# Optimization experiments

Hardware: AMD Instinct MI355X
Metric: run time of the kernel (lower is better)

Reference implementation:

```python
import jax, jax.numpy as jnp
import numpy as np

N_PFAS, N_GW, N_SW = 20000, 100000, 20000
D_IN, D_OUT = 64, 128
E_PG, E_GP, E_SP, E_PS = 1600000, 1600000, 400000, 400000


def setup_inputs() -> dict:
    key = jax.random.key(0)
    ks = jax.random.split(key, 32)
    nrm = lambda k, shp, s=1.0: jax.random.normal(k, shp, jnp.float32) * s
    W = 0.05  # weight init scale
    inp = {
        # node features
        "x_pfas": nrm(ks[0], (N_PFAS, D_IN)),
        "x_gw": nrm(ks[1], (N_GW, D_IN)),
        "x_sw": nrm(ks[2], (N_SW, D_IN)),
        # edge indices per relation (src, dst)
        "ei_pg_src": jax.random.randint(ks[3], (E_PG,), 0, N_PFAS),
        "ei_pg_dst": jax.random.randint(ks[4], (E_PG,), 0, N_GW),
        "ei_gp_src": jax.random.randint(ks[5], (E_GP,), 0, N_GW),
        "ei_gp_dst": jax.random.randint(ks[6], (E_GP,), 0, N_PFAS),
        "ei_sp_src": jax.random.randint(ks[7], (E_SP,), 0, N_SW),
        "ei_sp_dst": jax.random.randint(ks[8], (E_SP,), 0, N_PFAS),
        "ei_ps_src": jax.random.randint(ks[9], (E_PS,), 0, N_PFAS),
        "ei_ps_dst": jax.random.randint(ks[10], (E_PS,), 0, N_SW),
        # SAGEConv params per relation: lin_l (neighbors, with bias), lin_r (root, no bias)
        "Wl_pg": nrm(ks[11], (D_IN, D_OUT), W), "Wr_pg": nrm(ks[12], (D_IN, D_OUT), W), "b_pg": jnp.zeros((D_OUT,), jnp.float32),
        "Wl_gp": nrm(ks[13], (D_IN, D_OUT), W), "Wr_gp": nrm(ks[14], (D_IN, D_OUT), W), "b_gp": jnp.zeros((D_OUT,), jnp.float32),
        "Wl_sp": nrm(ks[15], (D_IN, D_OUT), W), "Wr_sp": nrm(ks[16], (D_IN, D_OUT), W), "b_sp": jnp.zeros((D_OUT,), jnp.float32),
        "Wl_ps": nrm(ks[17], (D_IN, D_OUT), W), "Wr_ps": nrm(ks[18], (D_IN, D_OUT), W), "b_ps": jnp.zeros((D_OUT,), jnp.float32),
        # final linear head + PReLU
        "W_lin": nrm(ks[19], (D_OUT, 1), W), "b_lin": jnp.zeros((1,), jnp.float32),
        "alpha": jnp.full((1,), 0.25, jnp.float32),
    }
    return inp


def _sage(x_src, x_dst, src, dst, Wl, Wr, b, n_dst):
    # PyG SAGEConv: out = lin_l(mean_{j in N(i)} x_j) + lin_r(x_i)
    msg = x_src[src]                                   # [E, D_in] gather
    agg = jax.ops.segment_sum(msg, dst, num_segments=n_dst)        # [n_dst, D_in]
    cnt = jax.ops.segment_sum(jnp.ones(src.shape, x_src.dtype), dst, num_segments=n_dst)
    mean = agg / jnp.maximum(cnt, 1.0)[:, None]
    return mean @ Wl + x_dst @ Wr + b


def _prelu(y, a):
    return jnp.where(y > 0, y, a * y)


def reference(x_pfas, x_gw, x_sw, ei_pg_src, ei_pg_dst, ei_gp_src, ei_gp_dst,
              ei_sp_src, ei_sp_dst, ei_ps_src, ei_ps_dst,
              Wl_pg, Wr_pg, b_pg, Wl_gp, Wr_gp, b_gp, Wl_sp, Wr_sp, b_sp,
              Wl_ps, Wr_ps, b_ps, W_lin, b_lin, alpha):
    # HeteroConv with aggr='sum': pfas_sites receives from two relations (summed)
    h_gw = jax.nn.relu(_sage(x_pfas, x_gw, ei_pg_src, ei_pg_dst, Wl_pg, Wr_pg, b_pg, N_GW))
    h_pfas = jax.nn.relu(
        _sage(x_gw, x_pfas, ei_gp_src, ei_gp_dst, Wl_gp, Wr_gp, b_gp, N_PFAS)
        + _sage(x_sw, x_pfas, ei_sp_src, ei_sp_dst, Wl_sp, Wr_sp, b_sp, N_PFAS))
    h_sw = jax.nn.relu(_sage(x_pfas, x_sw, ei_ps_src, ei_ps_dst, Wl_ps, Wr_ps, b_ps, N_SW))
    out_gw = _prelu(h_gw @ W_lin + b_lin, alpha)   # [N_GW, 1]
    out_sw = _prelu(h_sw @ W_lin + b_lin, alpha)   # [N_SW, 1]
    return (h_pfas, out_gw, out_sw)
```

## Files before the change

### kernel.cpp

```cpp
#include <hip/hip_runtime.h>
#include <hip/hip_bf16.h>

#define N_PFAS 20000
#define N_GW   100000
#define N_SW   20000
#define N_SEG  160000
#define BASE_GW 0
#define BASE_GP 100000
#define BASE_SP 120000
#define BASE_PS 140000
#define NBIN 1250
#define NB_FILL 512
#define SORT_CAP 12288
#define STAGE_CAP 8192
#define N_XROW 140000

typedef __attribute__((ext_vector_type(8))) short short8;
typedef __attribute__((ext_vector_type(4))) float f32x4;
typedef __attribute__((ext_vector_type(2))) float f32x2;

__device__ __forceinline__ unsigned short f2bf(float f) {
    union { float f; unsigned int u; } v;
    v.f = f;
    unsigned int u = v.u;
    unsigned int r = (u + 0x7fffu + ((u >> 16) & 1u)) >> 16;
    return (unsigned short)r;
}

#if __has_builtin(__builtin_amdgcn_cvt_pk_f32_fp8) && __has_builtin(__builtin_amdgcn_cvt_pk_fp8_f32)
#define FP8_HW 1
__device__ __forceinline__ unsigned int enc_fp8x4(float4 v) {
    int r = __builtin_amdgcn_cvt_pk_fp8_f32(v.x, v.y, 0, false);
    r = __builtin_amdgcn_cvt_pk_fp8_f32(v.z, v.w, r, true);
    return (unsigned int)r;
}
__device__ __forceinline__ void dec_fp8x4v(unsigned int u, f32x2& lo, f32x2& hi) {
    lo = __builtin_amdgcn_cvt_pk_f32_fp8(u, false);
    hi = __builtin_amdgcn_cvt_pk_f32_fp8(u, true);
}
#else
__device__ __forceinline__ unsigned char enc1_e5m2(float f) {
    union { unsigned short u; _Float16 h; } cv;
    cv.h = (_Float16)f;
    unsigned int u = cv.u;
    unsigned int r = (u + 0x7Fu + ((u >> 8) & 1u)) >> 8;
    return (unsigned char)(r > 255u ? 255u : r);
}
__device__ __forceinline__ unsigned int enc_fp8x4(float4 v) {
    return (unsigned int)enc1_e5m2(v.x) | ((unsigned int)enc1_e5m2(v.y) << 8)
         | ((unsigned int)enc1_e5m2(v.z) << 16) | ((unsigned int)enc1_e5m2(v.w) << 24);
}
__device__ __forceinline__ float dec1_e5m2(unsigned int b) {
    union { unsigned short u; _Float16 h; } cv;
    cv.u = (unsigned short)(b << 8);
    return (float)cv.h;
}
__device__ __forceinline__ void dec_fp8x4v(unsigned int u, f32x2& lo, f32x2& hi) {
    lo.x = dec1_e5m2(u & 0xFF); lo.y = dec1_e5m2((u >> 8) & 0xFF);
    hi.x = dec1_e5m2((u >> 16) & 0xFF); hi.y = dec1_e5m2(u >> 24);
}
#endif

__device__ __forceinline__ void edge_lookup(int i,
    const int* __restrict__ s0, const int* __restrict__ d0, int E0,
    const int* __restrict__ s1, const int* __restrict__ d1, int E1,
    const int* __restrict__ s2, const int* __restrict__ d2, int E2,
    const int* __restrict__ s3, const int* __restrict__ d3,
    int& g, int& sv)
{
    if (i < E0)                { g = BASE_GW + d0[i];                 sv = s0 ? s0[i] : 0; }
    else if (i < E0 + E1)      { int j = i - E0;           g = BASE_GP + d1[j]; sv = s1 ? s1[j] : 0; }
    else if (i < E0 + E1 + E2) { int j = i - E0 - E1;      g = BASE_SP + d2[j]; sv = s2 ? s2[j] : 0; }
    else                       { int j = i - E0 - E1 - E2; g = BASE_PS + d3[j]; sv = s3 ? s3[j] : 0; }
}

__global__ void __launch_bounds__(1024)
count_cast(const int* __restrict__ d0, int E0, const int* __restrict__ d1, int E1,
           const int* __restrict__ d2, int E2, const int* __restrict__ d3, int E3,
           const float* __restrict__ xp, const float* __restrict__ xg,
           const float* __restrict__ xs, unsigned short* __restrict__ x16,
           unsigned int* __restrict__ x8, int* __restrict__ countMat)
{
    const int T0 = 20000 * 16, T1 = 120000 * 16, TT = N_XROW * 16;
    for (int i = blockIdx.x * 1024 + threadIdx.x; i < TT; i += NB_FILL * 1024) {
        float4 v;
        if (i < T0)      v = ((const float4*)xp)[i];
        else if (i < T1) v = ((const float4*)xg)[i - T0];
        else             v = ((const float4*)xs)[i - T1];
        ushort4 o;
        o.x = f2bf(v.x); o.y = f2bf(v.y); o.z = f2bf(v.z); o.w = f2bf(v.w);
        ((ushort4*)x16)[i] = o;
        x8[i] = enc_fp8x4(v);
    }

    __shared__ int h[4][NBIN];
    for (int i = threadIdx.x; i < NBIN; i += 1024) {
        h[0][i] = 0; h[1][i] = 0; h[2][i] = 0; h[3][i] = 0;
    }
    __syncthreads();
    int sub = threadIdx.x & 3;
    int total = E0 + E1 + E2 + E3;
    int CH = (total + NB_FILL - 1) / NB_FILL;
    int s = blockIdx.x * CH;
    int e = s + CH; if (e > total) e = total;
    for (int i0 = s + threadIdx.x * 4; i0 < e; i0 += 1024 * 4) {
        int gs[4];
        int m = e - i0; if (m > 4) m = 4;
        #pragma unroll
        for (int u = 0; u < 4; u++) {
            if (u < m) {
                int g, sv;
                edge_lookup(i0 + u, nullptr, d0, E0, nullptr, d1, E1,
                            nullptr, d2, E2, nullptr, d3, g, sv);
                gs[u] = g;
            }
        }
        #pragma unroll
        for (int u = 0; u < 4; u++)
            if (u < m) atomicAdd(&h[sub][gs[u] >> 7], 1);
    }
    __syncthreads();
    for (int i = threadIdx.x; i < NBIN; i += 1024)
        countMat[blockIdx.x * NBIN + i] = h[0][i] + h[1][i] + h[2][i] + h[3][i];
}

__global__ void __launch_bounds__(1024)
scan_rows(const int* __restrict__ countMat, int* __restrict__ lofs)
{
    __shared__ int lds[2048];
    int k = blockIdx.x;
    int t = threadIdx.x;
    int v0 = (t < NBIN) ? countMat[k * NBIN + t] : 0;
    int v1 = (t + 1024 < NBIN) ? countMat[k * NBIN + t + 1024] : 0;
    lds[t] = v0; lds[t + 1024] = v1;
    __syncthreads();
    #pragma unroll
    for (int off = 1; off < 2048; off <<= 1) {
        int a = (t >= off) ? lds[t - off] : 0;
        int b = (t + 1024 >= off) ? lds[t + 1024 - off] : 0;
        __syncthreads();
        lds[t] += a; lds[t + 1024] += b;
        __syncthreads();
    }
    if (t < NBIN) lofs[k * NBIN + t] = lds[t] - v0;
    if (t + 1024 < NBIN) lofs[k * NBIN + t + 1024] = lds[t + 1024] - v1;
}

__global__ void __launch_bounds__(1024)
fill_stage(const int* __restrict__ s0, const int* __restrict__ d0, int E0,
           const int* __restrict__ s1, const int* __restrict__ d1, int E1,
           const int* __restrict__ s2, const int* __restrict__ d2, int E2,
           const int* __restrict__ s3, const int* __restrict__ d3, int E3,
           const int* __restrict__ lofs, int* __restrict__ eb)
{
    __shared__ int cur[NBIN];
    __shared__ int stage[STAGE_CAP];
    int k = blockIdx.x;
    for (int i = threadIdx.x; i < NBIN; i += 1024) cur[i] = lofs[k * NBIN + i];
    __syncthreads();
    int total = E0 + E1 + E2 + E3;
    int CH = (total + NB_FILL - 1) / NB_FILL;
    int s = k * CH;
    int e = s + CH; if (e > total) e = total;
    for (int i0 = s + threadIdx.x * 4; i0 < e; i0 += 1024 * 4) {
        int g[4], sv[4];
        int m = e - i0; if (m > 4) m = 4;
        #pragma unroll
        for (int u = 0; u < 4; u++)
            if (u < m) edge_lookup(i0 + u, s0, d0, E0, s1, d1, E1,
                                   s2, d2, E2, s3, d3, g[u], sv[u]);
        #pragma unroll
        for (int u = 0; u < 4; u++) {
            if (u < m) {
                int slot = atomicAdd(&cur[g[u] >> 7], 1);
                stage[slot] = sv[u] | ((g[u] & 127) << 20);
            }
        }
    }
    __syncthreads();
    int n = e - s;
    for (int i = threadIdx.x; i < n; i += 1024) eb[s + i] = stage[i];
}

__global__ void __launch_bounds__(1024)
sort_agg(const int* __restrict__ countMat, const int* __restrict__ lofs,
         const int* __restrict__ eb, const unsigned int* __restrict__ x8,
         unsigned short* __restrict__ meanAll, int E_total)
{
    __shared__ int stage[SORT_CAP];
    __shared__ unsigned short perm[SORT_CAP];
    __shared__ int rs[NB_FILL];
    __shared__ int cposS[NB_FILL + 1];
    __shared__ int cnt[128], basep[128], cur[128], lstart[128];
    int lane = threadIdx.x & 63;
    int t = threadIdx.x;
    int b = (int)((blockIdx.x + 781u) % NBIN);
    int CH = (E_total + NB_FILL - 1) / NB_FILL;

    if (t < 128) cnt[t] = 0;
    if (t < NB_FILL) {
        int ckv = countMat[t * NBIN + b];
        rs[t] = t * CH + lofs[t * NBIN + b];
        cposS[t + 1] = ckv;
    }
    if (t == 0) cposS[0] = 0;
    __syncthreads();
    #pragma unroll
    for (int off = 1; off < NB_FILL; off <<= 1) {
        int v = 0;
        if (t < NB_FILL && t >= off) v = cposS[t + 1 - off];
        __syncthreads();
        if (t < NB_FILL) cposS[t + 1] += v;
        __syncthreads();
    }
    int n = cposS[NB_FILL];
    if (n > SORT_CAP) n = SORT_CAP;

    for (int i = t; i < n; i += 1024) {
        int lo = 0, hi = NB_FILL;
        #pragma unroll
        for (int it = 0; it < 9; it++) {
            int mid = (lo + hi) >> 1;
            if (cposS[mid] <= i) lo = mid; else hi = mid;
        }
        int w = eb[rs[lo] + i - cposS[lo]];
        int dl = w >> 20;
        int g = (b << 7) + dl;
        int rb = (g < BASE_GP) ? 0 : (g < BASE_SP) ? 20000
               : (g < BASE_PS) ? 120000 : 0;
        stage[i] = ((w & 0xFFFFF) + rb) | (dl << 20);
        atomicAdd(&cnt[dl], 1);
    }
    __syncthreads();
    if (t < 128) basep[t] = cnt[t];
    __syncthreads();
    #pragma unroll
    for (int off = 1; off < 128; off <<= 1) {
        int v = 0;
        if (t < 128 && t >= off) v = basep[t - off];
        __syncthreads();
        if (t < 128) basep[t] += v;
        __syncthreads();
    }
    if (t < 128) {
        int ex = basep[t] - cnt[t];
        cur[t] = ex;
        lstart[t] = ex;
    }
    __syncthreads();

    for (int i = t; i < n; i += 1024) {
        int dl = stage[i] >> 20;
        int slot = atomicAdd(&cur[dl], 1);
        perm[slot] = (unsigned short)i;
    }
    __syncthreads();

    int wv = threadIdx.x >> 6;
    int h  = lane >> 5;
    int eq = (lane >> 3) & 3;
    int fc = lane & 7;
    int l32 = lane & 31;
    for (int it = 0; it < 4; it++) {
        int nl = 2 * (it * 16 + wv) + h;
        int s0 = lstart[nl];
        int c0 = cnt[nl];
        if (s0 + c0 > SORT_CAP) c0 = SORT_CAP - s0;
        f32x2 a01 = {0.f,0.f}, a23 = {0.f,0.f}, a45 = {0.f,0.f}, a67 = {0.f,0.f};
        int j = 0;
        for (; j + 32 <= c0; j += 32) {
            int ev = stage[perm[s0 + j + l32]] & 0xFFFFF;
            #pragma unroll
            for (int q = 0; q < 8; q++) {
                int id = __shfl(ev, h * 32 + 4 * q + eq);
                uint2 v = *(const uint2*)(x8 + (((size_t)id) << 4) + fc * 2);
                f32x2 lo0, hi0, lo1, hi1;
                dec_fp8x4v(v.x, lo0, hi0);
                dec_fp8x4v(v.y, lo1, hi1);
                a01 += lo0; a23 += hi0; a45 += lo1; a67 += hi1;
            }
        }
        if (j < c0) {
            int blk = c0 - j;
            int ev = (l32 < blk) ? (stage[perm[s0 + j + l32]] & 0xFFFFF) : 0;
            int ng = (blk + 3) >> 2;
            for (int q = 0; q < ng; q++) {
                int idx = 4 * q + eq;
                int id = __shfl(ev, h * 32 + idx);
                if (idx < blk) {
                    uint2 v = *(const uint2*)(x8 + (((size_t)id) << 4) + fc * 2);
                    f32x2 lo0, hi0, lo1, hi1;
                    dec_fp8x4v(v.x, lo0, hi0);
                    dec_fp8x4v(v.y, lo1, hi1);
                    a01 += lo0; a23 += hi0; a45 += lo1; a67 += hi1;
                }
            }
        }
        float f[8] = {a01.x, a01.y, a23.x, a23.y, a45.x, a45.y, a67.x, a67.y};
        #pragma unroll
        for (int r = 0; r < 8; r++) {
            f[r] += __shfl_xor(f[r], 8);
            f[r] += __shfl_xor(f[r], 16);
        }
        if (eq == 0) {
            float inv = 1.0f / (float)(c0 > 1 ? c0 : 1);
            ushort4 o0, o1;
            o0.x = f2bf(f[0] * inv); o0.y = f2bf(f[1] * inv);
            o0.z = f2bf(f[2] * inv); o0.w = f2bf(f[3] * inv);
            o1.x = f2bf(f[4] * inv); o1.y = f2bf(f[5] * inv);
            o1.z = f2bf(f[6] * inv); o1.w = f2bf(f[7] * inv);
            int gnode = (b << 7) + nl;
            ushort4* dst = (ushort4*)(meanAll + (size_t)gnode * 64 + fc * 8);
            dst[0] = o0;
            dst[1] = o1;
        }
    }
}

__device__ __forceinline__ void
head_body(const unsigned short* __restrict__ x16r,
          const unsigned short* __restrict__ mean,
          const float* __restrict__ Wl, const float* __restrict__ Wr,
          const float* __restrict__ b, const float* __restrict__ Wlin,
          const float* __restrict__ b_lin, const float* __restrict__ alpha,
          float* __restrict__ out, int N, int bid, int nblocks,
          unsigned short* __restrict__ smem)
{
    unsigned short* sW = smem;

    for (int i = threadIdx.x; i < 64 * 128; i += 256) {
        int k = i >> 7, col = i & 127;
        sW[col * 136 + k]      = f2bf(Wl[k * 128 + col]);
        sW[col * 136 + 64 + k] = f2bf(Wr[k * 128 + col]);
    }

    int lane = threadIdx.x & 63;
    int wid  = threadIdx.x >> 6;
    int c    = lane & 15;
    int quad = lane >> 4;
    float wl_c[8], b_c[8];
    #pragma unroll
    for (int t = 0; t < 8; t++) {
        wl_c[t] = Wlin[t * 16 + c];
        b_c[t]  = b[t * 16 + c];
    }
    float blin = b_lin[0], al = alpha[0];
    __syncthreads();

    int ntiles = (N + 63) >> 6;
    for (int tile = bid; tile < ntiles; tile += nblocks) {
        int base = tile << 6;
        int node = base + wid * 16 + c;
        bool valid = node < N;
        const unsigned short* mrow = mean + (size_t)node * 64;
        const unsigned short* xrow = x16r + (size_t)node * 64;

        f32x4 acc[8] = {};
        #pragma unroll
        for (int step = 0; step < 4; step++) {
            short8 a = {};
            if (valid) {
                const unsigned short* src = (step < 2)
                    ? (mrow + step * 32 + quad * 8)
                    : (xrow + (step - 2) * 32 + quad * 8);
                a = *(const short8*)src;
            }
            #pragma unroll
            for (int t = 0; t < 8; t++) {
                short8 bb = *(const short8*)&sW[(t * 16 + c) * 136 + step * 32 + quad * 8];
                acc[t] = __builtin_amdgcn_mfma_f32_16x16x32_bf16(a, bb, acc[t], 0, 0, 0);
            }
        }

        float p[4] = {0.f, 0.f, 0.f, 0.f};
        #pragma unroll
        for (int t = 0; t < 8; t++) {
            #pragma unroll
            for (int r = 0; r < 4; r++) {
                float h = fmaxf(acc[t][r] + b_c[t], 0.0f);
                p[r] += h * wl_c[t];
            }
        }
        #pragma unroll
        for (int m = 1; m < 16; m <<= 1) {
            #pragma unroll
            for (int r = 0; r < 4; r++) p[r] += __shfl_xor(p[r], m);
        }
        if (c == 0) {
            #pragma unroll
            for (int r = 0; r < 4; r++) {
                int onode = base + wid * 16 + quad * 4 + r;
                if (onode < N) {
                    float y = p[r] + blin;
                    out[onode] = y > 0.0f ? y : al * y;
                }
            }
        }
    }
}

__device__ __forceinline__ void
pfas_body(const unsigned short* __restrict__ x16p,
          const unsigned short* __restrict__ meanGP,
          const unsigned short* __restrict__ meanSP,
          const float* __restrict__ WlGP, const float* __restrict__ WrGP,
          const float* __restrict__ bGP,
          const float* __restrict__ WlSP, const float* __restrict__ WrSP,
          const float* __restrict__ bSP,
          float* __restrict__ out, int N, int bid, int nblocks,
          unsigned short* __restrict__ smem)
{
    unsigned short* sW = smem;

    for (int i = threadIdx.x; i < 64 * 128; i += 256) {
        int k = i >> 7, col = i & 127;
        sW[col * 200 + k]       = f2bf(WlGP[k * 128 + col]);
        sW[col * 200 + 64 + k]  = f2bf(WlSP[k * 128 + col]);
        sW[col * 200 + 128 + k] = f2bf(WrGP[k * 128 + col] + WrSP[k * 128 + col]);
    }

    int lane = threadIdx.x & 63;
    int wid  = threadIdx.x >> 6;
    int c    = lane & 15;
    int quad = lane >> 4;
    int rg   = (wid & 1) * 16;
    int cg   = (wid >> 1) * 4;
    float b_c[4];
    #pragma unroll
    for (int t = 0; t < 4; t++)
        b_c[t] = bGP[(cg + t) * 16 + c] + bSP[(cg + t) * 16 + c];
    __syncthreads();

    int ntiles = (N + 31) >> 5;
    for (int tile = bid; tile < ntiles; tile += nblocks) {
        int base = tile << 5;
        int node = base + rg + c;
        bool valid = node < N;
        const unsigned short* grow = meanGP + (size_t)node * 64;
        const unsigned short* srow = meanSP + (size_t)node * 64;
        const unsigned short* xrow = x16p + (size_t)node * 64;

        f32x4 acc[4] = {};
        #pragma unroll
        for (int step = 0; step < 6; step++) {
            short8 a = {};
            if (valid) {
                const unsigned short* src = (step < 2)
                    ? (grow + step * 32 + quad * 8)
                    : (step < 4) ? (srow + (step - 2) * 32 + quad * 8)
                                 : (xrow + (step - 4) * 32 + quad * 8);
                a = *(const short8*)src;
            }
            #pragma unroll
            for (int t = 0; t < 4; t++) {
                short8 bb = *(const short8*)&sW[((cg + t) * 16 + c) * 200 + step * 32 + quad * 8];
                acc[t] = __builtin_amdgcn_mfma_f32_16x16x32_bf16(a, bb, acc[t], 0, 0, 0);
            }
        }

        #pragma unroll
        for (int t = 0; t < 4; t++) {
            int col = (cg + t) * 16 + c;
            #pragma unroll
            for (int r = 0; r < 4; r++) {
                int onode = base + rg + quad * 4 + r;
                if (onode < N) {
                    float h = fmaxf(acc[t][r] + b_c[t], 0.0f);
                    out[(size_t)onode * 128 + col] = h;
                }
            }
        }
    }
}

__global__ void __launch_bounds__(256)
node_mfma(const unsigned short* __restrict__ x16,
          const unsigned short* __restrict__ meanAll,
          const float* __restrict__ Wl_pg, const float* __restrict__ Wr_pg,
          const float* __restrict__ b_pg,
          const float* __restrict__ Wl_ps, const float* __restrict__ Wr_ps,
          const float* __restrict__ b_ps,
          const float* __restrict__ Wl_gp, const float* __restrict__ Wr_gp,
          const float* __restrict__ b_gp,
          const float* __restrict__ Wl_sp, const float* __restrict__ Wr_sp,
          const float* __restrict__ b_sp,
          const float* __restrict__ W_lin, const float* __restrict__ b_lin,
          const float* __restrict__ alpha,
          float* __restrict__ out_gw, float* __restrict__ out_sw,
          float* __restrict__ out_pfas)
{
    __shared__ __align__(16) unsigned short smem[25600];
    int bx = blockIdx.x;
    if (bx < 512) {
        head_body(x16 + (size_t)20000 * 64, meanAll + (size_t)BASE_GW * 64,
                  Wl_pg, Wr_pg, b_pg, W_lin, b_lin, alpha,
                  out_gw, N_GW, bx, 512, smem);
    } else if (bx < 672) {
        head_body(x16 + (size_t)120000 * 64, meanAll + (size_t)BASE_PS * 64,
                  Wl_ps, Wr_ps, b_ps, W_lin, b_lin, alpha,
                  out_sw, N_SW, bx - 512, 160, smem);
    } else {
        pfas_body(x16, meanAll + (size_t)BASE_GP * 64, meanAll + (size_t)BASE_SP * 64,
                  Wl_gp, Wr_gp, b_gp, Wl_sp, Wr_sp, b_sp,
                  out_pfas, N_PFAS, bx - 672, 224, smem);
    }
}

extern "C" void kernel_launch(void* const* d_in, const int* in_sizes, int n_in,
                              void* d_out, int out_size, void* d_ws, size_t ws_size,
                              hipStream_t stream)
{
    const float* x_pfas = (const float*)d_in[0];
    const float* x_gw   = (const float*)d_in[1];
    const float* x_sw   = (const float*)d_in[2];
    const int* pg_src = (const int*)d_in[3];
    const int* pg_dst = (const int*)d_in[4];
    const int* gp_src = (const int*)d_in[5];
    const int* gp_dst = (const int*)d_in[6];
    const int* sp_src = (const int*)d_in[7];
    const int* sp_dst = (const int*)d_in[8];
    const int* ps_src = (const int*)d_in[9];
    const int* ps_dst = (const int*)d_in[10];
    const float* Wl_pg = (const float*)d_in[11];
    const float* Wr_pg = (const float*)d_in[12];
    const float* b_pg  = (const float*)d_in[13];
    const float* Wl_gp = (const float*)d_in[14];
    const float* Wr_gp = (const float*)d_in[15];
    const float* b_gp  = (const float*)d_in[16];
    const float* Wl_sp = (const float*)d_in[17];
    const float* Wr_sp = (const float*)d_in[18];
    const float* b_sp  = (const float*)d_in[19];
    const float* Wl_ps = (const float*)d_in[20];
    const float* Wr_ps = (const float*)d_in[21];
    const float* b_ps  = (const float*)d_in[22];
    const float* W_lin = (const float*)d_in[23];
    const float* b_lin = (const float*)d_in[24];
    const float* alpha = (const float*)d_in[25];

    float* out = (float*)d_out;
    float* out_pfas = out;
    float* out_gw   = out + (size_t)N_PFAS * 128;
    float* out_sw   = out_gw + N_GW;

    int E_PG = in_sizes[3];
    int E_GP = in_sizes[5];
    int E_SP = in_sizes[7];
    int E_PS = in_sizes[9];
    int E_total = E_PG + E_GP + E_SP + E_PS;

    unsigned short* meanAll = (unsigned short*)d_ws;
    int* countMat  = (int*)(meanAll + (size_t)N_SEG * 64);
    int* lofs      = countMat + NB_FILL * NBIN;
    int* edge_binned = lofs + NB_FILL * NBIN;
    unsigned short* x16 = (unsigned short*)(edge_binned + E_total);
    unsigned int* x8 = (unsigned int*)(x16 + (size_t)N_XROW * 64);

    count_cast<<<NB_FILL, 1024, 0, stream>>>(pg_dst, E_PG, gp_dst, E_GP,
                                             sp_dst, E_SP, ps_dst, E_PS,
                                             x_pfas, x_gw, x_sw, x16, x8,
                                             countMat);

    scan_rows<<<NB_FILL, 1024, 0, stream>>>(countMat, lofs);

    fill_stage<<<NB_FILL, 1024, 0, stream>>>(pg_src, pg_dst, E_PG,
                                             gp_src, gp_dst, E_GP,
                                             sp_src, sp_dst, E_SP,
                                             ps_src, ps_dst, E_PS,
                                             lofs, edge_binned);

    sort_agg<<<NBIN, 1024, 0, stream>>>(countMat, lofs, edge_binned,
                                        x8, meanAll, E_total);

    node_mfma<<<896, 256, 0, stream>>>(x16, meanAll,
                                       Wl_pg, Wr_pg, b_pg,
                                       Wl_ps, Wr_ps, b_ps,
                                       Wl_gp, Wr_gp, b_gp,
                                       Wl_sp, Wr_sp, b_sp,
                                       W_lin, b_lin, alpha,
                                       out_gw, out_sw, out_pfas);
}
```

Measured before the change: 270.3 us.

## Fuse row scan into fill_stage, transpose count tables, XCC-aware bin scheduling

The separate scan_rows kernel is removed. Its per-block prefix scan now runs at the start of fill_stage, which saves one launch and one round trip through global memory. A new transpose kernel writes countMat and lofs column-major, so sort_agg can read each bin's 512 entries contiguously instead of with a stride of NBIN. sort_agg now takes its bin from two atomic work queues chosen by XCC ID: XCCs 0-2 take the gp bins (781-936) and the others take the remaining bins, each falling back to the other queue when its own is empty. The aim is to keep the gp-relation bins on the same XCCs for L2 locality; the cost is an extra transpose launch and atomic dispatch per block.

```diff
diff --git a/kernel.cpp b/kernel.cpp
--- a/kernel.cpp
+++ b/kernel.cpp
@@ -14,6 +14,8 @@
 #define SORT_CAP 12288
 #define STAGE_CAP 8192
 #define N_XROW 140000
+#define N_GPQ 156
+#define N_OTQ 1094
 
 typedef __attribute__((ext_vector_type(8))) short short8;
 typedef __attribute__((ext_vector_type(4))) float f32x4;
@@ -125,39 +127,36 @@
 }
 
 __global__ void __launch_bounds__(1024)
-scan_rows(const int* __restrict__ countMat, int* __restrict__ lofs)
-{
-    __shared__ int lds[2048];
-    int k = blockIdx.x;
-    int t = threadIdx.x;
-    int v0 = (t < NBIN) ? countMat[k * NBIN + t] : 0;
-    int v1 = (t + 1024 < NBIN) ? countMat[k * NBIN + t + 1024] : 0;
-    lds[t] = v0; lds[t + 1024] = v1;
-    __syncthreads();
-    #pragma unroll
-    for (int off = 1; off < 2048; off <<= 1) {
-        int a = (t >= off) ? lds[t - off] : 0;
-        int b = (t + 1024 >= off) ? lds[t + 1024 - off] : 0;
-        __syncthreads();
-        lds[t] += a; lds[t + 1024] += b;
-        __syncthreads();
-    }
-    if (t < NBIN) lofs[k * NBIN + t] = lds[t] - v0;
-    if (t + 1024 < NBIN) lofs[k * NBIN + t + 1024] = lds[t + 1024] - v1;
-}
-
-__global__ void __launch_bounds__(1024)
 fill_stage(const int* __restrict__ s0, const int* __restrict__ d0, int E0,
            const int* __restrict__ s1, const int* __restrict__ d1, int E1,
            const int* __restrict__ s2, const int* __restrict__ d2, int E2,
            const int* __restrict__ s3, const int* __restrict__ d3, int E3,
-           const int* __restrict__ lofs, int* __restrict__ eb)
+           const int* __restrict__ countMat, int* __restrict__ lofs,
+           int* __restrict__ eb, int* __restrict__ qcnt)
 {
     __shared__ int cur[NBIN];
+    __shared__ int scanb[2048];
     __shared__ int stage[STAGE_CAP];
     int k = blockIdx.x;
-    for (int i = threadIdx.x; i < NBIN; i += 1024) cur[i] = lofs[k * NBIN + i];
-    __syncthreads();
+    int t = threadIdx.x;
+
+    int v0 = (t < NBIN) ? countMat[k * NBIN + t] : 0;
+    int v1 = (t + 1024 < NBIN) ? countMat[k * NBIN + t + 1024] : 0;
+    scanb[t] = v0; scanb[t + 1024] = v1;
+    __syncthreads();
+    #pragma unroll
+    for (int off = 1; off < 2048; off <<= 1) {
+        int a = (t >= off) ? scanb[t - off] : 0;
+        int b2 = (t + 1024 >= off) ? scanb[t + 1024 - off] : 0;
+        __syncthreads();
+        scanb[t] += a; scanb[t + 1024] += b2;
+        __syncthreads();
+    }
+    if (t < NBIN)        { int ex = scanb[t] - v0;        cur[t] = ex;        lofs[k * NBIN + t] = ex; }
+    if (t + 1024 < NBIN) { int ex = scanb[t + 1024] - v1; cur[t + 1024] = ex; lofs[k * NBIN + t + 1024] = ex; }
+    if (k == 0 && t < 2) qcnt[t] = 0;
+    __syncthreads();
+
     int total = E0 + E1 + E2 + E3;
     int CH = (total + NB_FILL - 1) / NB_FILL;
     int s = k * CH;
@@ -183,7 +182,29 @@
 }
 
 __global__ void __launch_bounds__(1024)
-sort_agg(const int* __restrict__ countMat, const int* __restrict__ lofs,
+transp(const int* __restrict__ cm, const int* __restrict__ lf,
+       int* __restrict__ cmT, int* __restrict__ lfT)
+{
+    __shared__ int t0[32][33], t1[32][33];
+    int tx = threadIdx.x & 31, ty = threadIdx.x >> 5;
+    int c = blockIdx.x * 32 + tx;
+    int r = blockIdx.y * 32 + ty;
+    if (c < NBIN) {
+        t0[ty][tx] = cm[r * NBIN + c];
+        t1[ty][tx] = lf[r * NBIN + c];
+    }
+    __syncthreads();
+    int c2 = blockIdx.x * 32 + ty;
+    int r2 = blockIdx.y * 32 + tx;
+    if (c2 < NBIN) {
+        cmT[c2 * NB_FILL + r2] = t0[tx][ty];
+        lfT[c2 * NB_FILL + r2] = t1[tx][ty];
+    }
+}
+
+__global__ void __launch_bounds__(1024)
+sort_agg(const int* __restrict__ cm, const int* __restrict__ lf,
+         int sA, int sB, int* __restrict__ qcnt,
          const int* __restrict__ eb, const unsigned int* __restrict__ x8,
          unsigned short* __restrict__ meanAll, int E_total)
 {
@@ -192,15 +213,39 @@
     __shared__ int rs[NB_FILL];
     __shared__ int cposS[NB_FILL + 1];
     __shared__ int cnt[128], basep[128], cur[128], lstart[128];
+    __shared__ int sbin;
     int lane = threadIdx.x & 63;
     int t = threadIdx.x;
-    int b = (int)((blockIdx.x + 781u) % NBIN);
     int CH = (E_total + NB_FILL - 1) / NB_FILL;
+
+    if (t == 0) {
+        unsigned xcc = (unsigned)__builtin_amdgcn_s_getreg((31 << 11) | 20) & 0xfu;
+        int pref = (xcc < 3u) ? 0 : 1;
+        int bsel = -1;
+        int idx = atomicAdd(&qcnt[pref], 1);
+        if (pref == 0) {
+            if (idx < N_GPQ) bsel = 781 + idx;
+            else {
+                int j = atomicAdd(&qcnt[1], 1);
+                if (j < N_OTQ) bsel = (j < 781) ? j : (937 + (j - 781));
+            }
+        } else {
+            if (idx < N_OTQ) bsel = (idx < 781) ? idx : (937 + (idx - 781));
+            else {
+                int j = atomicAdd(&qcnt[0], 1);
+                if (j < N_GPQ) bsel = 781 + j;
+            }
+        }
+        sbin = bsel;
+    }
+    __syncthreads();
+    int b = sbin;
+    if (b < 0) return;
 
     if (t < 128) cnt[t] = 0;
     if (t < NB_FILL) {
-        int ckv = countMat[t * NBIN + b];
-        rs[t] = t * CH + lofs[t * NBIN + b];
+        int ckv = cm[t * sA + b * sB];
+        rs[t] = t * CH + lf[t * sA + b * sB];
         cposS[t + 1] = ckv;
     }
     if (t == 0) cposS[0] = 0;
@@ -551,25 +596,34 @@
     unsigned short* meanAll = (unsigned short*)d_ws;
     int* countMat  = (int*)(meanAll + (size_t)N_SEG * 64);
     int* lofs      = countMat + NB_FILL * NBIN;
-    int* edge_binned = lofs + NB_FILL * NBIN;
+    int* qcnt      = lofs + NB_FILL * NBIN;
+    int* edge_binned = qcnt + 8;
     unsigned short* x16 = (unsigned short*)(edge_binned + E_total);
     unsigned int* x8 = (unsigned int*)(x16 + (size_t)N_XROW * 64);
+    int* cmT = (int*)(x8 + (size_t)N_XROW * 16);
+    int* lfT = cmT + NB_FILL * NBIN;
+    size_t needT = (size_t)((char*)(lfT + NB_FILL * NBIN) - (char*)d_ws);
+    bool useT = (ws_size >= needT);
 
     count_cast<<<NB_FILL, 1024, 0, stream>>>(pg_dst, E_PG, gp_dst, E_GP,
                                              sp_dst, E_SP, ps_dst, E_PS,
                                              x_pfas, x_gw, x_sw, x16, x8,
                                              countMat);
 
-    scan_rows<<<NB_FILL, 1024, 0, stream>>>(countMat, lofs);
-
     fill_stage<<<NB_FILL, 1024, 0, stream>>>(pg_src, pg_dst, E_PG,
                                              gp_src, gp_dst, E_GP,
                                              sp_src, sp_dst, E_SP,
                                              ps_src, ps_dst, E_PS,
-                                             lofs, edge_binned);
-
-    sort_agg<<<NBIN, 1024, 0, stream>>>(countMat, lofs, edge_binned,
-                                        x8, meanAll, E_total);
+                                             countMat, lofs, edge_binned, qcnt);
+
+    if (useT) {
+        transp<<<dim3(40, 16), 1024, 0, stream>>>(countMat, lofs, cmT, lfT);
+        sort_agg<<<NBIN, 1024, 0, stream>>>(cmT, lfT, 1, NB_FILL, qcnt,
+                                            edge_binned, x8, meanAll, E_total);
+    } else {
+        sort_agg<<<NBIN, 1024, 0, stream>>>(countMat, lofs, NBIN, 1, qcnt,
+                                            edge_binned, x8, meanAll, E_total);
+    }
 
     node_mfma<<<896, 256, 0, stream>>>(x16, meanAll,
                                        Wl_pg, Wr_pg, b_pg,
```

New measurement: 297.2 us. 1.1x slower.
